# Performance work log

Hardware: AMD Instinct MI355X
Metric: run time of the kernel (lower is better)

Reference implementation:

```python
import jax, jax.numpy as jnp
import numpy as np

B, HID = 32768, 128
NU = 0.49                 # poisson_ratio default
LAM_PHYS, LAM_EL = 0.1, 0.05
EPS = 1e-7


def setup_inputs() -> dict:
    key = jax.random.key(0)
    ks = jax.random.split(key, 8)
    def w(k, shape, fan_in):
        return jax.random.normal(k, shape, jnp.float32) / np.float32(np.sqrt(fan_in))
    return {
        "coords": jax.random.normal(ks[0], (B, 3), jnp.float32),
        "target_labels": jax.random.uniform(ks[1], (B, 1), jnp.float32),
        "target_stiffness": jax.random.uniform(ks[2], (B, 1), jnp.float32) * 10.0,
        "W1": w(ks[3], (3, HID), 3), "b1": jnp.zeros((HID,), jnp.float32),
        "W2": w(ks[4], (HID, HID), HID), "b2": jnp.zeros((HID,), jnp.float32),
        "Wp": w(ks[5], (HID, 1), HID), "bp": jnp.zeros((1,), jnp.float32),
        "Ws": w(ks[6], (HID, 1), HID), "bs": jnp.zeros((1,), jnp.float32),
        "Wd": w(ks[7], (HID, 3), HID), "bd": jnp.zeros((3,), jnp.float32),
    }


def reference(coords, target_labels, target_stiffness,
              W1, b1, W2, b2, Wp, bp, Ws, bs, Wd, bd):
    def feats(x):  # x: (...,3) -> (...,HID)
        h = jnp.tanh(x @ W1 + b1)
        return jnp.tanh(h @ W2 + b2)

    h = feats(coords)                                   # (B,HID)
    prediction = jax.nn.sigmoid(h @ Wp + bp)            # (B,1)
    stiffness = jax.nn.softplus(h @ Ws + bs)            # (B,1) Young's modulus E

    # displacement field u(x): R^3 -> R^3, pointwise
    def disp_fn(x):  # (3,) -> (3,)
        return feats(x) @ Wd + bd

    # Per-point Hessian H[b,i,j,k] = d2 u_i / dx_j dx_k  (B,3,3,3)
    Hm = jax.vmap(jax.jacfwd(jax.jacfwd(disp_fn)))(coords)
    laplacian = jnp.einsum('bijj->bi', Hm)              # (B,3) lap(u_i)
    grad_div = jnp.einsum('biik->bk', Hm)               # (B,3) grad(div u)

    # Lame parameters from E (matches torch code incl. nu_denom clamp)
    mu = stiffness / (2.0 * (1.0 + NU))
    nu_denom = max(1.0 - 2.0 * NU, 1e-5)
    lmbda = stiffness * NU / ((1.0 + NU) * nu_denom)
    residual = mu * laplacian + (lmbda + mu) * grad_div  # (B,3)
    phys_loss = jnp.mean(jnp.sum(residual ** 2, axis=-1))

    # BCE on clamped prediction/labels
    p = jnp.clip(prediction, EPS, 1.0 - EPS)
    t = jnp.clip(target_labels, 0.0, 1.0)
    bce = -jnp.mean(t * jnp.log(p) + (1.0 - t) * jnp.log(1.0 - p))
    data_loss = bce + 0.5 * jnp.mean((stiffness - target_stiffness) ** 2)

    elastic_loss = jnp.mean(jax.nn.relu(-stiffness) + jax.nn.relu(stiffness - 15.0))

    total = data_loss + LAM_PHYS * phys_loss + LAM_EL * elastic_loss
    raw_losses = jnp.stack([data_loss, phys_loss, elastic_loss])
    return total, raw_losses
```

## Files before the change

### kernel.cpp

```cpp
#include <hip/hip_runtime.h>
#include <math.h>

#define HIDN 128
#define NPTS 32768
#define PTS_PER_BLK 16
#define NBLK (NPTS / PTS_PER_BLK)

#define MU_COEF 0.33557046979865773f
#define LM_COEF 16.442953020134228f

typedef float f32x4  __attribute__((ext_vector_type(4)));
typedef short bf16x8 __attribute__((ext_vector_type(8)));


__device__ __forceinline__ unsigned short f2bf(float f) {
    unsigned u = __builtin_bit_cast(unsigned, f);
    u += 0x7fffu + ((u >> 16) & 1u);
    return (unsigned short)(u >> 16);
}

__device__ __forceinline__ float tanh_fast(float x) {
    float e = __builtin_amdgcn_exp2f(x * 2.885390081777927f);
    return 1.0f - 2.0f * __builtin_amdgcn_rcpf(e + 1.0f);
}

__global__ void prep_kernel(const float* __restrict__ W1,
                            const float* __restrict__ b1,
                            const float* __restrict__ W2,
                            float* __restrict__ ws)
{
    float* accum = ws;
    float* tab   = ws + 128;
    unsigned short* W2bf = (unsigned short*)(ws + 2048);
    int tid = blockIdx.x * blockDim.x + threadIdx.x;
    if (tid < 8) accum[tid] = 0.0f;
    if (tid < HIDN) {
        float w0 = W1[0 * HIDN + tid];
        float w1 = W1[1 * HIDN + tid];
        float w2 = W1[2 * HIDN + tid];
        float* t = tab + tid * 12;
        t[0] = w0; t[1] = w1; t[2] = w2; t[3] = b1[tid];
        t[4] = w0 * w0; t[5] = w0 * w1; t[6] = w0 * w2;
        t[7] = w1 * w1; t[8] = w1 * w2; t[9] = w2 * w2;
        t[10] = 0.0f; t[11] = 0.0f;
    }
    for (int i = tid; i < HIDN * HIDN; i += gridDim.x * blockDim.x) {
        int m = i >> 7, h = i & 127;
        W2bf[m * HIDN + h] = f2bf(W2[h * HIDN + m]);
    }
}

__global__ __launch_bounds__(256, 3) void pinn_main(
    const float* __restrict__ coords,
    const float* __restrict__ labels,
    const float* __restrict__ tstiff,
    const float* __restrict__ b2,
    const float* __restrict__ Wp, const float* __restrict__ bp,
    const float* __restrict__ Wsv, const float* __restrict__ bs,
    const float* __restrict__ Wd,
    const float* __restrict__ ws_ro,
    float* __restrict__ accum)
{
    const float* tab = ws_ro + 128;
    const unsigned short* W2bf = (const unsigned short*)(ws_ro + 2048);

    __shared__ __align__(16) char smem[43584];
    unsigned short* A  = (unsigned short*)smem;
    float*          red  = (float*)smem;
    float*          red2 = (float*)(smem + 43520);

    const int tid  = threadIdx.x;
    const int wave = __builtin_amdgcn_readfirstlane(tid >> 6);
    const int lane = tid & 63;
    const int blk  = blockIdx.x;

    {
        const int b  = tid & 15;
        const int hc = tid >> 4;
        const int h0 = hc * 8;
        const int gb = blk * PTS_PER_BLK + b;
        const float x0 = coords[gb * 3 + 0];
        const float x1 = coords[gb * 3 + 1];
        const float x2 = coords[gb * 3 + 2];
        unsigned pk[10][4];
#pragma unroll
        for (int i = 0; i < 8; ++i) {
            const float* t = tab + (h0 + i) * 12;
            float z = fmaf(x0, t[0], fmaf(x1, t[1], fmaf(x2, t[2], t[3])));
            float a  = tanh_fast(z);
            float g  = fmaf(-a, a, 1.0f);
            float ag = a * g;
            float c[10];
            c[0] = a;
            c[1] = g * t[0]; c[2] = g * t[1]; c[3] = g * t[2];
            c[4] = ag * t[4]; c[5] = ag * t[5]; c[6] = ag * t[6];
            c[7] = ag * t[7]; c[8] = ag * t[8]; c[9] = ag * t[9];
#pragma unroll
            for (int ch = 0; ch < 10; ++ch) {
                unsigned v = f2bf(c[ch]);
                if ((i & 1) == 0) pk[ch][i >> 1] = v;
                else              pk[ch][i >> 1] |= v << 16;
            }
        }
#pragma unroll
        for (int ch = 0; ch < 10; ++ch) {
            uint4* dst = (uint4*)(A + ch * (16 * 136) + b * 136 + h0);
            *dst = make_uint4(pk[ch][0], pk[ch][1], pk[ch][2], pk[ch][3]);
        }
    }
    __syncthreads();

    const int l = lane & 15;
    const int q = lane >> 4;

    f32x4 acc[10][2] = {};
#pragma unroll
    for (int ks = 0; ks < 4; ++ks) {
        const int hk = ks * 32 + q * 8;
        bf16x8 bfr[2];
#pragma unroll
        for (int mt = 0; mt < 2; ++mt) {
            const int m = wave * 32 + mt * 16 + l;
            bfr[mt] = *(const bf16x8*)(W2bf + m * HIDN + hk);
        }
#pragma unroll
        for (int ch = 0; ch < 10; ++ch) {
            bf16x8 afr = *(const bf16x8*)(A + ch * (16 * 136) + l * 136 + hk);
            acc[ch][0] = __builtin_amdgcn_mfma_f32_16x16x32_bf16(afr, bfr[0], acc[ch][0], 0, 0, 0);
            acc[ch][1] = __builtin_amdgcn_mfma_f32_16x16x32_bf16(afr, bfr[1], acc[ch][1], 0, 0, 0);
        }
    }

    float sum[4][8] = {};
#pragma unroll
    for (int mt = 0; mt < 2; ++mt) {
        const int m = wave * 32 + mt * 16 + l;
        const float wd0 = Wd[m * 3 + 0];
        const float wd1 = Wd[m * 3 + 1];
        const float wd2 = Wd[m * 3 + 2];
        const float wp  = Wp[m];
        const float wsv = Wsv[m];
        const float b2v = b2[m];
#pragma unroll
        for (int r = 0; r < 4; ++r) {
            const float z2 = acc[0][mt][r] + b2v;
            const float a2 = tanh_fast(z2);
            const float g2 = fmaf(-a2, a2, 1.0f);
            const float d2 = -2.0f * a2 * g2;
            const float t0 = acc[1][mt][r], t1 = acc[2][mt][r], t2 = acc[3][mt][r];
            const float q00 = acc[4][mt][r], q01 = acc[5][mt][r], q02 = acc[6][mt][r];
            const float q11 = acc[7][mt][r], q12 = acc[8][mt][r], q22 = acc[9][mt][r];
            const float qtr = q00 + q11 + q22;
            const float tt  = t0 * t0 + t1 * t1 + t2 * t2;
            const float Lm  = fmaf(-2.0f * g2, qtr, d2 * tt);
            const float wt  = wd0 * t0 + wd1 * t1 + wd2 * t2;
            const float m2g2 = -2.0f * g2;
            const float dwt  = d2 * wt;
            const float r0 = wd0 * q00 + wd1 * q01 + wd2 * q02;
            const float r1 = wd0 * q01 + wd1 * q11 + wd2 * q12;
            const float r2 = wd0 * q02 + wd1 * q12 + wd2 * q22;
            sum[r][0] += wp  * a2;
            sum[r][1] += wsv * a2;
            sum[r][2] += wd0 * Lm;
            sum[r][3] += wd1 * Lm;
            sum[r][4] += wd2 * Lm;
            sum[r][5] += m2g2 * r0 + dwt * t0;
            sum[r][6] += m2g2 * r1 + dwt * t1;
            sum[r][7] += m2g2 * r2 + dwt * t2;
        }
    }
    __syncthreads();

#pragma unroll
    for (int r = 0; r < 4; ++r) {
        const int b = q * 4 + r;
        const int slot = wave * 16 + l;
        float4* dst = (float4*)(red + (b * 64 + slot) * 8);
        dst[0] = make_float4(sum[r][0], sum[r][1], sum[r][2], sum[r][3]);
        dst[1] = make_float4(sum[r][4], sum[r][5], sum[r][6], sum[r][7]);
    }
    __syncthreads();

    {
        const int b  = tid >> 4;
        const int l2 = tid & 15;
        float v[8] = {};
#pragma unroll
        for (int w = 0; w < 4; ++w) {
            const float4* src = (const float4*)(red + (b * 64 + w * 16 + l2) * 8);
            float4 p0 = src[0], p1 = src[1];
            v[0] += p0.x; v[1] += p0.y; v[2] += p0.z; v[3] += p0.w;
            v[4] += p1.x; v[5] += p1.y; v[6] += p1.z; v[7] += p1.w;
        }
#pragma unroll
        for (int k = 0; k < 8; ++k) {
            v[k] += __shfl_xor(v[k], 1);
            v[k] += __shfl_xor(v[k], 2);
            v[k] += __shfl_xor(v[k], 4);
            v[k] += __shfl_xor(v[k], 8);
        }
        float bce_t = 0.f, sq_t = 0.f, phys_t = 0.f, el_t = 0.f;
        if (l2 == 0) {
            const int gb = blk * PTS_PER_BLK + b;
            const float fzp = v[0] + bp[0];
            const float fzs = v[1] + bs[0];
            float pred = 1.0f / (1.0f + expf(-fzp));
            pred = fminf(fmaxf(pred, 1e-7f), 1.0f - 1e-7f);
            const float E = fmaxf(fzs, 0.0f) + log1pf(expf(-fabsf(fzs)));
            const float mu = E * MU_COEF;
            const float cc = E * LM_COEF + mu;
            const float rr0 = mu * v[2] + cc * v[5];
            const float rr1 = mu * v[3] + cc * v[6];
            const float rr2 = mu * v[4] + cc * v[7];
            phys_t = rr0 * rr0 + rr1 * rr1 + rr2 * rr2;
            float tl = labels[gb];
            tl = fminf(fmaxf(tl, 0.0f), 1.0f);
            bce_t = -(tl * logf(pred) + (1.0f - tl) * logf(1.0f - pred));
            const float dsv = E - tstiff[gb];
            sq_t = dsv * dsv;
            el_t = fmaxf(-E, 0.0f) + fmaxf(E - 15.0f, 0.0f);
        }
#pragma unroll
        for (int m = 16; m < 64; m <<= 1) {
            bce_t  += __shfl_xor(bce_t, m);
            sq_t   += __shfl_xor(sq_t, m);
            phys_t += __shfl_xor(phys_t, m);
            el_t   += __shfl_xor(el_t, m);
        }
        if (lane == 0) {
            red2[wave * 4 + 0] = bce_t;
            red2[wave * 4 + 1] = sq_t;
            red2[wave * 4 + 2] = phys_t;
            red2[wave * 4 + 3] = el_t;
        }
    }
    __syncthreads();
    if (tid < 4) {
        float s = red2[0 * 4 + tid] + red2[1 * 4 + tid] + red2[2 * 4 + tid] + red2[3 * 4 + tid];
        atomicAdd(accum + tid, s);
    }
}

__global__ void finalize_kernel(const float* __restrict__ accum,
                                float* __restrict__ out)
{
    if (threadIdx.x == 0 && blockIdx.x == 0) {
        const float invB = 1.0f / (float)NPTS;
        const float bce  = accum[0] * invB;
        const float data = bce + 0.5f * accum[1] * invB;
        const float phys = accum[2] * invB;
        const float el   = accum[3] * invB;
        out[0] = data + 0.1f * phys + 0.05f * el;
        out[1] = data;
        out[2] = phys;
        out[3] = el;
    }
}

extern "C" void kernel_launch(void* const* d_in, const int* in_sizes, int n_in,
                              void* d_out, int out_size, void* d_ws, size_t ws_size,
                              hipStream_t stream)
{
    const float* coords = (const float*)d_in[0];
    const float* labels = (const float*)d_in[1];
    const float* tstiff = (const float*)d_in[2];
    const float* W1  = (const float*)d_in[3];
    const float* b1  = (const float*)d_in[4];
    const float* W2  = (const float*)d_in[5];
    const float* b2  = (const float*)d_in[6];
    const float* Wp  = (const float*)d_in[7];
    const float* bp  = (const float*)d_in[8];
    const float* Wsv = (const float*)d_in[9];
    const float* bs  = (const float*)d_in[10];
    const float* Wd  = (const float*)d_in[11];

    float* ws  = (float*)d_ws;
    float* out = (float*)d_out;

    prep_kernel<<<64, 256, 0, stream>>>(W1, b1, W2, ws);
    pinn_main<<<NBLK, 256, 0, stream>>>(coords, labels, tstiff, b2,
                                        Wp, bp, Wsv, bs, Wd, ws, ws);
    finalize_kernel<<<1, 64, 0, stream>>>(ws, out);
}
```

Before: 116.4 us.

## Transpose MFMA operands so each lane holds one point, shrinking the epilogue reduction

Swaps the A/B operands of the MFMA so the accumulator layout puts points on lanes and hidden units on registers. Each lane then sums over its hidden units in registers, replacing the large shared-memory staging and 16-lane shuffle reduction with two shuffles and a small LDS buffer. Per-unit weights (Wd, Wp, Ws, b2) are packed by the prep kernel into one table that each block loads into LDS. Shared memory per block grows, which may limit occupancy, and the final atomics are now issued by a single lane.

```diff
diff --git a/kernel.cpp b/kernel.cpp
--- a/kernel.cpp
+++ b/kernel.cpp
@@ -27,11 +27,16 @@
 __global__ void prep_kernel(const float* __restrict__ W1,
                             const float* __restrict__ b1,
                             const float* __restrict__ W2,
+                            const float* __restrict__ Wd,
+                            const float* __restrict__ Wp,
+                            const float* __restrict__ Wsv,
+                            const float* __restrict__ b2,
                             float* __restrict__ ws)
 {
     float* accum = ws;
     float* tab   = ws + 128;
     unsigned short* W2bf = (unsigned short*)(ws + 2048);
+    float* mtab  = ws + 10240;
     int tid = blockIdx.x * blockDim.x + threadIdx.x;
     if (tid < 8) accum[tid] = 0.0f;
     if (tid < HIDN) {
@@ -43,6 +48,10 @@
         t[4] = w0 * w0; t[5] = w0 * w1; t[6] = w0 * w2;
         t[7] = w1 * w1; t[8] = w1 * w2; t[9] = w2 * w2;
         t[10] = 0.0f; t[11] = 0.0f;
+        float* mt = mtab + tid * 8;
+        mt[0] = Wd[tid * 3 + 0]; mt[1] = Wd[tid * 3 + 1]; mt[2] = Wd[tid * 3 + 2];
+        mt[3] = Wp[tid]; mt[4] = Wsv[tid]; mt[5] = b2[tid];
+        mt[6] = 0.0f; mt[7] = 0.0f;
     }
     for (int i = tid; i < HIDN * HIDN; i += gridDim.x * blockDim.x) {
         int m = i >> 7, h = i & 127;
@@ -54,25 +63,31 @@
     const float* __restrict__ coords,
     const float* __restrict__ labels,
     const float* __restrict__ tstiff,
-    const float* __restrict__ b2,
-    const float* __restrict__ Wp, const float* __restrict__ bp,
-    const float* __restrict__ Wsv, const float* __restrict__ bs,
-    const float* __restrict__ Wd,
+    const float* __restrict__ bp,
+    const float* __restrict__ bs,
     const float* __restrict__ ws_ro,
     float* __restrict__ accum)
 {
     const float* tab = ws_ro + 128;
     const unsigned short* W2bf = (const unsigned short*)(ws_ro + 2048);
-
-    __shared__ __align__(16) char smem[43584];
-    unsigned short* A  = (unsigned short*)smem;
-    float*          red  = (float*)smem;
-    float*          red2 = (float*)(smem + 43520);
+    const float* ws_mtab = ws_ro + 10240;
+
+    __shared__ __align__(16) char smem[49664];
+    unsigned short* A     = (unsigned short*)smem;
+    float*          mtabL = (float*)(smem + 43520);
+    float*          red2b = (float*)(smem + 47616);
 
     const int tid  = threadIdx.x;
     const int wave = __builtin_amdgcn_readfirstlane(tid >> 6);
     const int lane = tid & 63;
     const int blk  = blockIdx.x;
+
+    if (tid < 128) {
+        const f32x4 m0 = *(const f32x4*)(ws_mtab + tid * 8);
+        const f32x4 m1 = *(const f32x4*)(ws_mtab + tid * 8 + 4);
+        *(f32x4*)(mtabL + tid * 8)     = m0;
+        *(f32x4*)(mtabL + tid * 8 + 4) = m1;
+    }
 
     {
         const int b  = tid & 15;
@@ -126,23 +141,21 @@
 #pragma unroll
         for (int ch = 0; ch < 10; ++ch) {
             bf16x8 afr = *(const bf16x8*)(A + ch * (16 * 136) + l * 136 + hk);
-            acc[ch][0] = __builtin_amdgcn_mfma_f32_16x16x32_bf16(afr, bfr[0], acc[ch][0], 0, 0, 0);
-            acc[ch][1] = __builtin_amdgcn_mfma_f32_16x16x32_bf16(afr, bfr[1], acc[ch][1], 0, 0, 0);
-        }
-    }
-
-    float sum[4][8] = {};
+            acc[ch][0] = __builtin_amdgcn_mfma_f32_16x16x32_bf16(bfr[0], afr, acc[ch][0], 0, 0, 0);
+            acc[ch][1] = __builtin_amdgcn_mfma_f32_16x16x32_bf16(bfr[1], afr, acc[ch][1], 0, 0, 0);
+        }
+    }
+
+    float sum[8] = {0, 0, 0, 0, 0, 0, 0, 0};
 #pragma unroll
     for (int mt = 0; mt < 2; ++mt) {
-        const int m = wave * 32 + mt * 16 + l;
-        const float wd0 = Wd[m * 3 + 0];
-        const float wd1 = Wd[m * 3 + 1];
-        const float wd2 = Wd[m * 3 + 2];
-        const float wp  = Wp[m];
-        const float wsv = Wsv[m];
-        const float b2v = b2[m];
 #pragma unroll
         for (int r = 0; r < 4; ++r) {
+            const int m = wave * 32 + mt * 16 + q * 4 + r;
+            const f32x4 mw0 = *(const f32x4*)(mtabL + m * 8);
+            const f32x4 mw1 = *(const f32x4*)(mtabL + m * 8 + 4);
+            const float wd0 = mw0[0], wd1 = mw0[1], wd2 = mw0[2], wpv = mw0[3];
+            const float wsv = mw1[0], b2v = mw1[1];
             const float z2 = acc[0][mt][r] + b2v;
             const float a2 = tanh_fast(z2);
             const float g2 = fmaf(-a2, a2, 1.0f);
@@ -152,92 +165,76 @@
             const float q11 = acc[7][mt][r], q12 = acc[8][mt][r], q22 = acc[9][mt][r];
             const float qtr = q00 + q11 + q22;
             const float tt  = t0 * t0 + t1 * t1 + t2 * t2;
-            const float Lm  = fmaf(-2.0f * g2, qtr, d2 * tt);
+            const float m2g2 = -2.0f * g2;
+            const float Lm  = fmaf(m2g2, qtr, d2 * tt);
             const float wt  = wd0 * t0 + wd1 * t1 + wd2 * t2;
-            const float m2g2 = -2.0f * g2;
-            const float dwt  = d2 * wt;
+            const float dwt = d2 * wt;
             const float r0 = wd0 * q00 + wd1 * q01 + wd2 * q02;
             const float r1 = wd0 * q01 + wd1 * q11 + wd2 * q12;
             const float r2 = wd0 * q02 + wd1 * q12 + wd2 * q22;
-            sum[r][0] += wp  * a2;
-            sum[r][1] += wsv * a2;
-            sum[r][2] += wd0 * Lm;
-            sum[r][3] += wd1 * Lm;
-            sum[r][4] += wd2 * Lm;
-            sum[r][5] += m2g2 * r0 + dwt * t0;
-            sum[r][6] += m2g2 * r1 + dwt * t1;
-            sum[r][7] += m2g2 * r2 + dwt * t2;
-        }
+            sum[0] += wpv * a2;
+            sum[1] += wsv * a2;
+            sum[2] += wd0 * Lm;
+            sum[3] += wd1 * Lm;
+            sum[4] += wd2 * Lm;
+            sum[5] += m2g2 * r0 + dwt * t0;
+            sum[6] += m2g2 * r1 + dwt * t1;
+            sum[7] += m2g2 * r2 + dwt * t2;
+        }
+    }
+
+#pragma unroll
+    for (int k = 0; k < 8; ++k) {
+        sum[k] += __shfl_xor(sum[k], 16);
+        sum[k] += __shfl_xor(sum[k], 32);
+    }
+    if (lane < 16) {
+        float4* dst = (float4*)(red2b + (wave * 16 + lane) * 8);
+        dst[0] = make_float4(sum[0], sum[1], sum[2], sum[3]);
+        dst[1] = make_float4(sum[4], sum[5], sum[6], sum[7]);
     }
     __syncthreads();
 
-#pragma unroll
-    for (int r = 0; r < 4; ++r) {
-        const int b = q * 4 + r;
-        const int slot = wave * 16 + l;
-        float4* dst = (float4*)(red + (b * 64 + slot) * 8);
-        dst[0] = make_float4(sum[r][0], sum[r][1], sum[r][2], sum[r][3]);
-        dst[1] = make_float4(sum[r][4], sum[r][5], sum[r][6], sum[r][7]);
-    }
-    __syncthreads();
-
-    {
-        const int b  = tid >> 4;
-        const int l2 = tid & 15;
-        float v[8] = {};
+    if (tid < 16) {
+        float v[8] = {0, 0, 0, 0, 0, 0, 0, 0};
 #pragma unroll
         for (int w = 0; w < 4; ++w) {
-            const float4* src = (const float4*)(red + (b * 64 + w * 16 + l2) * 8);
-            float4 p0 = src[0], p1 = src[1];
+            const float4* src = (const float4*)(red2b + (w * 16 + tid) * 8);
+            const float4 p0 = src[0], p1 = src[1];
             v[0] += p0.x; v[1] += p0.y; v[2] += p0.z; v[3] += p0.w;
             v[4] += p1.x; v[5] += p1.y; v[6] += p1.z; v[7] += p1.w;
         }
-#pragma unroll
-        for (int k = 0; k < 8; ++k) {
-            v[k] += __shfl_xor(v[k], 1);
-            v[k] += __shfl_xor(v[k], 2);
-            v[k] += __shfl_xor(v[k], 4);
-            v[k] += __shfl_xor(v[k], 8);
-        }
-        float bce_t = 0.f, sq_t = 0.f, phys_t = 0.f, el_t = 0.f;
-        if (l2 == 0) {
-            const int gb = blk * PTS_PER_BLK + b;
-            const float fzp = v[0] + bp[0];
-            const float fzs = v[1] + bs[0];
-            float pred = 1.0f / (1.0f + expf(-fzp));
-            pred = fminf(fmaxf(pred, 1e-7f), 1.0f - 1e-7f);
-            const float E = fmaxf(fzs, 0.0f) + log1pf(expf(-fabsf(fzs)));
-            const float mu = E * MU_COEF;
-            const float cc = E * LM_COEF + mu;
-            const float rr0 = mu * v[2] + cc * v[5];
-            const float rr1 = mu * v[3] + cc * v[6];
-            const float rr2 = mu * v[4] + cc * v[7];
-            phys_t = rr0 * rr0 + rr1 * rr1 + rr2 * rr2;
-            float tl = labels[gb];
-            tl = fminf(fmaxf(tl, 0.0f), 1.0f);
-            bce_t = -(tl * logf(pred) + (1.0f - tl) * logf(1.0f - pred));
-            const float dsv = E - tstiff[gb];
-            sq_t = dsv * dsv;
-            el_t = fmaxf(-E, 0.0f) + fmaxf(E - 15.0f, 0.0f);
-        }
-#pragma unroll
-        for (int m = 16; m < 64; m <<= 1) {
-            bce_t  += __shfl_xor(bce_t, m);
-            sq_t   += __shfl_xor(sq_t, m);
-            phys_t += __shfl_xor(phys_t, m);
-            el_t   += __shfl_xor(el_t, m);
-        }
-        if (lane == 0) {
-            red2[wave * 4 + 0] = bce_t;
-            red2[wave * 4 + 1] = sq_t;
-            red2[wave * 4 + 2] = phys_t;
-            red2[wave * 4 + 3] = el_t;
-        }
-    }
-    __syncthreads();
-    if (tid < 4) {
-        float s = red2[0 * 4 + tid] + red2[1 * 4 + tid] + red2[2 * 4 + tid] + red2[3 * 4 + tid];
-        atomicAdd(accum + tid, s);
+        const int gb = blk * PTS_PER_BLK + tid;
+        const float fzp = v[0] + bp[0];
+        const float fzs = v[1] + bs[0];
+        float pred = 1.0f / (1.0f + expf(-fzp));
+        pred = fminf(fmaxf(pred, 1e-7f), 1.0f - 1e-7f);
+        const float E = fmaxf(fzs, 0.0f) + log1pf(expf(-fabsf(fzs)));
+        const float mu = E * MU_COEF;
+        const float cc = E * LM_COEF + mu;
+        const float rr0 = mu * v[2] + cc * v[5];
+        const float rr1 = mu * v[3] + cc * v[6];
+        const float rr2 = mu * v[4] + cc * v[7];
+        float phys_t = rr0 * rr0 + rr1 * rr1 + rr2 * rr2;
+        float tl = labels[gb];
+        tl = fminf(fmaxf(tl, 0.0f), 1.0f);
+        float bce_t = -(tl * logf(pred) + (1.0f - tl) * logf(1.0f - pred));
+        const float dsv = E - tstiff[gb];
+        float sq_t = dsv * dsv;
+        float el_t = fmaxf(-E, 0.0f) + fmaxf(E - 15.0f, 0.0f);
+#pragma unroll
+        for (int mk = 1; mk < 16; mk <<= 1) {
+            bce_t  += __shfl_xor(bce_t, mk);
+            sq_t   += __shfl_xor(sq_t, mk);
+            phys_t += __shfl_xor(phys_t, mk);
+            el_t   += __shfl_xor(el_t, mk);
+        }
+        if (tid == 0) {
+            atomicAdd(accum + 0, bce_t);
+            atomicAdd(accum + 1, sq_t);
+            atomicAdd(accum + 2, phys_t);
+            atomicAdd(accum + 3, el_t);
+        }
     }
 }
 
@@ -277,8 +274,7 @@
     float* ws  = (float*)d_ws;
     float* out = (float*)d_out;
 
-    prep_kernel<<<64, 256, 0, stream>>>(W1, b1, W2, ws);
-    pinn_main<<<NBLK, 256, 0, stream>>>(coords, labels, tstiff, b2,
-                                        Wp, bp, Wsv, bs, Wd, ws, ws);
+    prep_kernel<<<64, 256, 0, stream>>>(W1, b1, W2, Wd, Wp, Wsv, b2, ws);
+    pinn_main<<<NBLK, 256, 0, stream>>>(coords, labels, tstiff, bp, bs, ws, ws);
     finalize_kernel<<<1, 64, 0, stream>>>(ws, out);
 }
```

New measurement: 191.9 us. 1.65x slower.

## Fold Wd into second-layer weights to cut Hessian channels from ten to eight

Applied to the files above, without the earlier changes.

The six per-unit second-derivative channels are replaced by two kinds of channel: a trace channel that uses the precomputed squared norm of the W1 row, and three channels multiplied by a new precomputed bf16 matrix W2*(W1·Wd). The main kernel then runs 8 channels of MFMA instead of 10, and the per-point epilogue no longer contracts q with Wd. Shared memory also shrinks, and the wider table load is vectorized. In exchange, the prep kernel builds one more 128x128 bf16 matrix, and folding Wd before the bf16 rounding changes where precision is lost.

```diff
diff --git a/kernel.cpp b/kernel.cpp
--- a/kernel.cpp
+++ b/kernel.cpp
@@ -5,6 +5,7 @@
 #define NPTS 32768
 #define PTS_PER_BLK 16
 #define NBLK (NPTS / PTS_PER_BLK)
+#define NCH 8
 
 #define MU_COEF 0.33557046979865773f
 #define LM_COEF 16.442953020134228f
@@ -27,26 +28,32 @@
 __global__ void prep_kernel(const float* __restrict__ W1,
                             const float* __restrict__ b1,
                             const float* __restrict__ W2,
+                            const float* __restrict__ Wd,
                             float* __restrict__ ws)
 {
     float* accum = ws;
     float* tab   = ws + 128;
     unsigned short* W2bf = (unsigned short*)(ws + 2048);
+    unsigned short* B2bf = (unsigned short*)(ws + 10240);
     int tid = blockIdx.x * blockDim.x + threadIdx.x;
     if (tid < 8) accum[tid] = 0.0f;
     if (tid < HIDN) {
         float w0 = W1[0 * HIDN + tid];
         float w1 = W1[1 * HIDN + tid];
         float w2 = W1[2 * HIDN + tid];
-        float* t = tab + tid * 12;
+        float* t = tab + tid * 8;
         t[0] = w0; t[1] = w1; t[2] = w2; t[3] = b1[tid];
-        t[4] = w0 * w0; t[5] = w0 * w1; t[6] = w0 * w2;
-        t[7] = w1 * w1; t[8] = w1 * w2; t[9] = w2 * w2;
-        t[10] = 0.0f; t[11] = 0.0f;
+        t[4] = w0 * w0 + w1 * w1 + w2 * w2;
+        t[5] = 0.0f; t[6] = 0.0f; t[7] = 0.0f;
     }
     for (int i = tid; i < HIDN * HIDN; i += gridDim.x * blockDim.x) {
-        int m = i >> 7, h = i & 127;
-        W2bf[m * HIDN + h] = f2bf(W2[h * HIDN + m]);
+        int h = i >> 7, m = i & 127;
+        float w2v = W2[i];
+        W2bf[m * HIDN + h] = f2bf(w2v);
+        float wdot = W1[0 * HIDN + h] * Wd[m * 3 + 0]
+                   + W1[1 * HIDN + h] * Wd[m * 3 + 1]
+                   + W1[2 * HIDN + h] * Wd[m * 3 + 2];
+        B2bf[m * HIDN + h] = f2bf(w2v * wdot);
     }
 }
 
@@ -63,11 +70,12 @@
 {
     const float* tab = ws_ro + 128;
     const unsigned short* W2bf = (const unsigned short*)(ws_ro + 2048);
-
-    __shared__ __align__(16) char smem[43584];
+    const unsigned short* B2bf = (const unsigned short*)(ws_ro + 10240);
+
+    __shared__ __align__(16) char smem[34880];
     unsigned short* A  = (unsigned short*)smem;
     float*          red  = (float*)smem;
-    float*          red2 = (float*)(smem + 43520);
+    float*          red2 = (float*)(smem + 34816);
 
     const int tid  = threadIdx.x;
     const int wave = __builtin_amdgcn_readfirstlane(tid >> 6);
@@ -82,28 +90,30 @@
         const float x0 = coords[gb * 3 + 0];
         const float x1 = coords[gb * 3 + 1];
         const float x2 = coords[gb * 3 + 2];
-        unsigned pk[10][4];
+        unsigned pk[NCH][4];
 #pragma unroll
         for (int i = 0; i < 8; ++i) {
-            const float* t = tab + (h0 + i) * 12;
-            float z = fmaf(x0, t[0], fmaf(x1, t[1], fmaf(x2, t[2], t[3])));
+            const float* t = tab + (h0 + i) * 8;
+            const f32x4 tv = *(const f32x4*)t;
+            const float ww = t[4];
+            float z = fmaf(x0, tv[0], fmaf(x1, tv[1], fmaf(x2, tv[2], tv[3])));
             float a  = tanh_fast(z);
             float g  = fmaf(-a, a, 1.0f);
             float ag = a * g;
-            float c[10];
+            float c[NCH];
             c[0] = a;
-            c[1] = g * t[0]; c[2] = g * t[1]; c[3] = g * t[2];
-            c[4] = ag * t[4]; c[5] = ag * t[5]; c[6] = ag * t[6];
-            c[7] = ag * t[7]; c[8] = ag * t[8]; c[9] = ag * t[9];
-#pragma unroll
-            for (int ch = 0; ch < 10; ++ch) {
+            c[1] = g * tv[0]; c[2] = g * tv[1]; c[3] = g * tv[2];
+            c[4] = ag * ww;
+            c[5] = a * c[1];  c[6] = a * c[2];  c[7] = a * c[3];
+#pragma unroll
+            for (int ch = 0; ch < NCH; ++ch) {
                 unsigned v = f2bf(c[ch]);
                 if ((i & 1) == 0) pk[ch][i >> 1] = v;
                 else              pk[ch][i >> 1] |= v << 16;
             }
         }
 #pragma unroll
-        for (int ch = 0; ch < 10; ++ch) {
+        for (int ch = 0; ch < NCH; ++ch) {
             uint4* dst = (uint4*)(A + ch * (16 * 136) + b * 136 + h0);
             *dst = make_uint4(pk[ch][0], pk[ch][1], pk[ch][2], pk[ch][3]);
         }
@@ -113,21 +123,28 @@
     const int l = lane & 15;
     const int q = lane >> 4;
 
-    f32x4 acc[10][2] = {};
+    f32x4 acc[NCH][2] = {};
 #pragma unroll
     for (int ks = 0; ks < 4; ++ks) {
         const int hk = ks * 32 + q * 8;
-        bf16x8 bfr[2];
+        bf16x8 bfr[2], cfr[2];
 #pragma unroll
         for (int mt = 0; mt < 2; ++mt) {
             const int m = wave * 32 + mt * 16 + l;
             bfr[mt] = *(const bf16x8*)(W2bf + m * HIDN + hk);
-        }
-#pragma unroll
-        for (int ch = 0; ch < 10; ++ch) {
+            cfr[mt] = *(const bf16x8*)(B2bf + m * HIDN + hk);
+        }
+#pragma unroll
+        for (int ch = 0; ch < 5; ++ch) {
             bf16x8 afr = *(const bf16x8*)(A + ch * (16 * 136) + l * 136 + hk);
             acc[ch][0] = __builtin_amdgcn_mfma_f32_16x16x32_bf16(afr, bfr[0], acc[ch][0], 0, 0, 0);
             acc[ch][1] = __builtin_amdgcn_mfma_f32_16x16x32_bf16(afr, bfr[1], acc[ch][1], 0, 0, 0);
+        }
+#pragma unroll
+        for (int ch = 5; ch < 8; ++ch) {
+            bf16x8 afr = *(const bf16x8*)(A + ch * (16 * 136) + l * 136 + hk);
+            acc[ch][0] = __builtin_amdgcn_mfma_f32_16x16x32_bf16(afr, cfr[0], acc[ch][0], 0, 0, 0);
+            acc[ch][1] = __builtin_amdgcn_mfma_f32_16x16x32_bf16(afr, cfr[1], acc[ch][1], 0, 0, 0);
         }
     }
 
@@ -148,17 +165,13 @@
             const float g2 = fmaf(-a2, a2, 1.0f);
             const float d2 = -2.0f * a2 * g2;
             const float t0 = acc[1][mt][r], t1 = acc[2][mt][r], t2 = acc[3][mt][r];
-            const float q00 = acc[4][mt][r], q01 = acc[5][mt][r], q02 = acc[6][mt][r];
-            const float q11 = acc[7][mt][r], q12 = acc[8][mt][r], q22 = acc[9][mt][r];
-            const float qtr = q00 + q11 + q22;
+            const float qtr = acc[4][mt][r];
+            const float r0 = acc[5][mt][r], r1 = acc[6][mt][r], r2 = acc[7][mt][r];
             const float tt  = t0 * t0 + t1 * t1 + t2 * t2;
-            const float Lm  = fmaf(-2.0f * g2, qtr, d2 * tt);
+            const float m2g2 = -2.0f * g2;
+            const float Lm  = fmaf(m2g2, qtr, d2 * tt);
             const float wt  = wd0 * t0 + wd1 * t1 + wd2 * t2;
-            const float m2g2 = -2.0f * g2;
             const float dwt  = d2 * wt;
-            const float r0 = wd0 * q00 + wd1 * q01 + wd2 * q02;
-            const float r1 = wd0 * q01 + wd1 * q11 + wd2 * q12;
-            const float r2 = wd0 * q02 + wd1 * q12 + wd2 * q22;
             sum[r][0] += wp  * a2;
             sum[r][1] += wsv * a2;
             sum[r][2] += wd0 * Lm;
@@ -277,7 +290,7 @@
     float* ws  = (float*)d_ws;
     float* out = (float*)d_out;
 
-    prep_kernel<<<64, 256, 0, stream>>>(W1, b1, W2, ws);
+    prep_kernel<<<64, 256, 0, stream>>>(W1, b1, W2, Wd, ws);
     pinn_main<<<NBLK, 256, 0, stream>>>(coords, labels, tstiff, b2,
                                         Wp, bp, Wsv, bs, Wd, ws, ws);
     finalize_kernel<<<1, 64, 0, stream>>>(ws, out);
```

New measurement: 120.1 us. +3.2%, slower.
